# Kernel tuning notes

Measured on AMD Instinct MI355X. Metric: run time of the kernel, lower is better.

The kernel has to match this reference:

```python
import jax, jax.numpy as jnp
import numpy as np

B, C, F, TP = 16, 64, 128, 100
E = 576
NFEAT, NHID, NOUT = 128, 128, 64
RATIO = 0.9
BN_EPS = 1e-5


def setup_inputs() -> dict:
    key = jax.random.key(0)
    ks = jax.random.split(key, 16)
    s = 0.05
    h = jax.random.normal(ks[0], (B, C, F, TP), jnp.float32)
    edge_index = jax.random.randint(ks[1], (2, E), 0, C, dtype=jnp.int32)
    edge_weight = jax.random.uniform(ks[2], (E,), jnp.float32)
    W1 = jax.random.normal(ks[3], (NFEAT, NHID), jnp.float32) / np.float32(np.sqrt(NFEAT))
    b1 = s * jax.random.normal(ks[4], (NHID,), jnp.float32)
    g1 = 1.0 + s * jax.random.normal(ks[5], (NHID,), jnp.float32)
    be1 = s * jax.random.normal(ks[6], (NHID,), jnp.float32)
    a1 = jnp.full((1,), 0.25, jnp.float32)  # PReLU slope
    Wp = jax.random.normal(ks[7], (NHID, 1), jnp.float32) / np.float32(np.sqrt(NHID))
    bp = s * jax.random.normal(ks[8], (1,), jnp.float32)
    W2 = jax.random.normal(ks[9], (NHID, NOUT), jnp.float32) / np.float32(np.sqrt(NHID))
    b2 = s * jax.random.normal(ks[10], (NOUT,), jnp.float32)
    g2 = 1.0 + s * jax.random.normal(ks[11], (NOUT,), jnp.float32)
    be2 = s * jax.random.normal(ks[12], (NOUT,), jnp.float32)
    a2 = jnp.full((1,), 0.25, jnp.float32)
    return dict(h=h, edge_index=edge_index, edge_weight=edge_weight,
                W1=W1, b1=b1, g1=g1, be1=be1, a1=a1, Wp=Wp, bp=bp,
                W2=W2, b2=b2, g2=g2, be2=be2, a2=a2)


def gcn_conv(x, W, b, row, col, ew, N):
    # PyG GCNConv: add self-loops (weight 1), symmetric normalization, x@W, scatter-add to col.
    si = jnp.arange(N, dtype=row.dtype)
    r = jnp.concatenate([row, si])
    c = jnp.concatenate([col, si])
    w = jnp.concatenate([ew, jnp.ones((N,), x.dtype)])
    deg = jax.ops.segment_sum(w, c, num_segments=N)
    dis = jnp.where(deg > 0, jax.lax.rsqrt(jnp.maximum(deg, 1e-12)), 0.0)
    norm = dis[r] * w * dis[c]
    hlin = x @ W
    out = jax.ops.segment_sum(hlin[r] * norm[:, None], c, num_segments=N)
    return out + b


def batchnorm(x, g, beta):
    m = jnp.mean(x, axis=0)
    v = jnp.mean((x - m) ** 2, axis=0)  # biased var, as in torch BN training
    return (x - m) * jax.lax.rsqrt(v + BN_EPS) * g + beta


def prelu(x, a):
    return jnp.where(x >= 0, x, a * x)


def reference(h, edge_index, edge_weight, W1, b1, g1, be1, a1, Wp, bp, W2, b2, g2, be2, a2):
    Bv, Cv, Fv, Tpv = h.shape
    G = Bv * Tpv                      # num_graphs
    N = G * Cv                        # total nodes
    K = int(np.ceil(RATIO * Cv))      # kept nodes per graph (static)
    x = jnp.transpose(h, (0, 3, 1, 2)).reshape(N, Fv)
    Ev = edge_index.shape[1]
    offs = jnp.repeat(jnp.arange(G, dtype=edge_index.dtype) * Cv, Ev)
    row = jnp.tile(edge_index[0], G) + offs
    col = jnp.tile(edge_index[1], G) + offs
    ew = jnp.tile(edge_weight, G)
    # gc1 -> bn1 -> prelu
    x = prelu(batchnorm(gcn_conv(x, W1, b1, row, col, ew, N), g1, be1), a1)
    # SAGPooling: score GNN (GCNConv, no edge weights), tanh, per-graph top-k
    score = jnp.tanh(gcn_conv(x, Wp, bp, row, col, jnp.ones_like(ew), N)[:, 0])
    topv, topi = jax.lax.top_k(score.reshape(G, Cv), K)
    perm = (topi + (jnp.arange(G, dtype=topi.dtype) * Cv)[:, None]).reshape(-1)
    xk = x[perm] * topv.reshape(-1)[:, None]
    Nk = G * K
    new_id = jnp.zeros((N,), jnp.int32).at[perm].set(jnp.arange(Nk, dtype=jnp.int32))
    kept = jnp.zeros((N,), bool).at[perm].set(True)
    valid = kept[row] & kept[col]
    r2 = new_id[row]
    c2 = new_id[col]
    w2 = jnp.where(valid, ew, 0.0)    # dropped edges: weight 0 == filtered out
    # gc2 -> bn2 -> prelu (dropout is identity in eval)
    x2 = prelu(batchnorm(gcn_conv(xk, W2, b2, r2, c2, w2, Nk), g2, be2), a2)
    # global mean pool: exactly K nodes per graph, contiguous
    z = x2.reshape(G, K, -1).mean(axis=1)
    z_seq = jnp.transpose(z.reshape(Bv, Tpv, -1), (0, 2, 1))
    return x2, z_seq
```

## Files before the change

### kernel.cpp

```cpp
#include <hip/hip_runtime.h>

constexpr int Bc   = 16;
constexpr int Cc   = 64;
constexpr int Fc   = 128;
constexpr int TPc  = 100;
constexpr int Gc   = Bc * TPc;
constexpr int Nc   = Gc * Cc;
constexpr int Ec   = 576;
constexpr int NHID = 128;
constexpr int NOUTc= 64;
constexpr int Kc   = 58;
constexpr int Nkc  = Gc * Kc;

__global__ void k0_prep(const int* __restrict__ ei, const float* __restrict__ ew,
                        float* __restrict__ A1, float* __restrict__ AP,
                        double* bn1S, double* bn1Q, double* bn2S, double* bn2Q) {
    __shared__ float deg1[64], degP[64], dis1[64], disP[64];
    __shared__ float A1L[4096], APL[4096];
    int t = threadIdx.x;
    if (t < 64) { deg1[t] = 1.0f; degP[t] = 1.0f; }
    for (int i = t; i < 4096; i += 256) { A1L[i] = 0.f; APL[i] = 0.f; }
    if (t < 128) { bn1S[t] = 0.0; bn1Q[t] = 0.0; }
    if (t < 64)  { bn2S[t] = 0.0; bn2Q[t] = 0.0; }
    __syncthreads();
    for (int e = t; e < Ec; e += 256) {
        int c = ei[Ec + e];
        atomicAdd(&deg1[c], ew[e]);
        atomicAdd(&degP[c], 1.0f);
    }
    __syncthreads();
    if (t < 64) { dis1[t] = 1.0f / sqrtf(deg1[t]); disP[t] = 1.0f / sqrtf(degP[t]); }
    __syncthreads();
    for (int e = t; e < Ec; e += 256) {
        int r = ei[e], c = ei[Ec + e];
        atomicAdd(&A1L[c * 64 + r], dis1[r] * ew[e] * dis1[c]);
        atomicAdd(&APL[c * 64 + r], disP[r] * disP[c]);
    }
    __syncthreads();
    if (t < 64) {
        A1L[t * 65] += dis1[t] * dis1[t];
        APL[t * 65] += disP[t] * disP[t];
    }
    __syncthreads();
    for (int i = t; i < 4096; i += 256) { A1[i] = A1L[i]; AP[i] = APL[i]; }
}

__global__ __launch_bounds__(256)
void k_trans(const float* __restrict__ h, float* __restrict__ XT) {
    __shared__ float tile[64 * 101];
    int blk = blockIdx.x;
    int b = blk >> 7, f = blk & 127;
    int t = threadIdx.x;
    const float* hb = h + (size_t)b * 819200 + (size_t)f * 100;
    for (int i = t; i < 6400; i += 256) {
        unsigned c = (unsigned)i / 100u;
        unsigned tp = (unsigned)i - c * 100u;
        tile[c * 101 + tp] = hb[(size_t)c * 12800 + tp];
    }
    __syncthreads();
    float* xb = XT + (size_t)b * 100 * 8192 + f * 64;
    for (int j = t; j < 6400; j += 256) {
        int tp = j >> 6, c = j & 63;
        xb[(size_t)tp * 8192 + c] = tile[c * 101 + tp];
    }
}

__global__ __launch_bounds__(256, 2)
void k1_gc1(const float* __restrict__ XT, const float* __restrict__ W1,
            const float* __restrict__ b1, const float* __restrict__ A1,
            float* __restrict__ Y1, double* bn1S, double* bn1Q) {
    __shared__ float XsT[128 * 64];
    __shared__ float WH [64 * 128];
    __shared__ float A1s[4096];
    int g = blockIdx.x;
    int t = threadIdx.x;
    int tx = t & 31, ty = t >> 5;

    {
        const float4* src = (const float4*)(XT + (size_t)g * 8192);
        float4* dst = (float4*)XsT;
#pragma unroll
        for (int it = 0; it < 8; ++it) dst[it * 256 + t] = src[it * 256 + t];
    }
    for (int i = t; i < 4096; i += 256) A1s[i] = A1[i];

    float acc[8][4];
#pragma unroll
    for (int i = 0; i < 8; ++i)
#pragma unroll
        for (int j = 0; j < 4; ++j) acc[i][j] = 0.f;

    for (int kh = 0; kh < 2; ++kh) {
        __syncthreads();
        for (int it = 0; it < 32; ++it) {
            int e2 = it * 256 + t;
            int f = e2 & 127, kk = e2 >> 7;
            WH[kk * 128 + f] = W1[(kh * 64 + kk) * 128 + f];
        }
        __syncthreads();
        for (int kk = 0; kk < 64; ++kk) {
            int k = kh * 64 + kk;
            float4 x0 = *(const float4*)&XsT[k * 64 + ty * 8];
            float4 x1 = *(const float4*)&XsT[k * 64 + ty * 8 + 4];
            float4 w  = *(const float4*)&WH[kk * 128 + tx * 4];
            float xr[8] = {x0.x, x0.y, x0.z, x0.w, x1.x, x1.y, x1.z, x1.w};
#pragma unroll
            for (int i = 0; i < 8; ++i) {
                acc[i][0] += xr[i] * w.x;
                acc[i][1] += xr[i] * w.y;
                acc[i][2] += xr[i] * w.z;
                acc[i][3] += xr[i] * w.w;
            }
        }
    }
    __syncthreads();
#pragma unroll
    for (int i = 0; i < 8; ++i) {
        float4 v = make_float4(acc[i][0], acc[i][1], acc[i][2], acc[i][3]);
        *(float4*)&WH[(ty * 8 + i) * 128 + tx * 4] = v;
    }
    __syncthreads();
    float acy[8][4];
    float4 bb = *(const float4*)&b1[tx * 4];
#pragma unroll
    for (int i = 0; i < 8; ++i) { acy[i][0] = bb.x; acy[i][1] = bb.y; acy[i][2] = bb.z; acy[i][3] = bb.w; }
    for (int rr = 0; rr < 16; ++rr) {
        float4 hrow[4];
#pragma unroll
        for (int q = 0; q < 4; ++q) hrow[q] = *(const float4*)&WH[(rr * 4 + q) * 128 + tx * 4];
#pragma unroll
        for (int i = 0; i < 8; ++i) {
            float4 a4 = *(const float4*)&A1s[(ty * 8 + i) * 64 + rr * 4];
            acy[i][0] += a4.x * hrow[0].x + a4.y * hrow[1].x + a4.z * hrow[2].x + a4.w * hrow[3].x;
            acy[i][1] += a4.x * hrow[0].y + a4.y * hrow[1].y + a4.z * hrow[2].y + a4.w * hrow[3].y;
            acy[i][2] += a4.x * hrow[0].z + a4.y * hrow[1].z + a4.z * hrow[2].z + a4.w * hrow[3].z;
            acy[i][3] += a4.x * hrow[0].w + a4.y * hrow[1].w + a4.z * hrow[2].w + a4.w * hrow[3].w;
        }
    }
    float ps[4] = {0, 0, 0, 0}, pq[4] = {0, 0, 0, 0};
    float* Yg = Y1 + (size_t)g * 64 * 128;
#pragma unroll
    for (int i = 0; i < 8; ++i) {
        float4 v = make_float4(acy[i][0], acy[i][1], acy[i][2], acy[i][3]);
        *(float4*)&Yg[(ty * 8 + i) * 128 + tx * 4] = v;
#pragma unroll
        for (int j = 0; j < 4; ++j) { ps[j] += acy[i][j]; pq[j] += acy[i][j] * acy[i][j]; }
    }
    float* redS = XsT;
    float* redQ = XsT + 1024;
#pragma unroll
    for (int j = 0; j < 4; ++j) {
        redS[ty * 128 + tx * 4 + j] = ps[j];
        redQ[ty * 128 + tx * 4 + j] = pq[j];
    }
    __syncthreads();
    if (t < 128) {
        float S = 0.f, Q = 0.f;
        for (int y = 0; y < 8; ++y) { S += redS[y * 128 + t]; Q += redQ[y * 128 + t]; }
        atomicAdd(&bn1S[t], (double)S);
        atomicAdd(&bn1Q[t], (double)Q);
    }
}

__global__ void k_bnfin(const double* __restrict__ S, const double* __restrict__ Q,
                        const float* __restrict__ gam, const float* __restrict__ bet,
                        float* __restrict__ scale, float* __restrict__ shift, double invN) {
    int t = threadIdx.x;
    double m = S[t] * invN;
    double v = Q[t] * invN - m * m;
    double rstd = 1.0 / sqrt(v + 1e-5);
    float sc = (float)((double)gam[t] * rstd);
    scale[t] = sc;
    shift[t] = bet[t] - (float)m * sc;
}

__global__ __launch_bounds__(256, 2)
void k3_pool_gc2(const float* __restrict__ Y1, const float* __restrict__ scale1,
                 const float* __restrict__ shift1, const float* __restrict__ a1,
                 const float* __restrict__ Wp, const float* __restrict__ bp,
                 const float* __restrict__ AP, const int* __restrict__ ei,
                 const float* __restrict__ ew, const float* __restrict__ W2,
                 const float* __restrict__ b2,
                 float* __restrict__ Y2, double* bn2S, double* bn2Q) {
    __shared__ float Xs[64 * 132];
    __shared__ float A2s[4096];
    __shared__ float H2s[64 * 66];
    __shared__ float slin[64], psum[256], score[64], dis2[64], deg2[64];
    __shared__ int   rnk[64], ord[64];
    int g = blockIdx.x, t = threadIdx.x;
    int tx = t & 31, ty = t >> 5;
    float alpha1 = a1[0];

    const float* Yg = Y1 + (size_t)g * 8192;
    for (int it = 0; it < 32; ++it) {
        int e = it * 256 + t;
        int f = e & 127, c = e >> 7;
        float v = Yg[e] * scale1[f] + shift1[f];
        v = (v >= 0.f) ? v : alpha1 * v;
        Xs[c * 132 + f] = v;
    }
    __syncthreads();
    {
        int rr = t >> 2, q4 = t & 3;
        float sp = 0.f;
        for (int m = 0; m < 32; ++m) sp += Xs[rr * 132 + q4 * 32 + m] * Wp[q4 * 32 + m];
        psum[t] = sp;
    }
    __syncthreads();
    if (t < 64) slin[t] = psum[t * 4] + psum[t * 4 + 1] + psum[t * 4 + 2] + psum[t * 4 + 3];
    __syncthreads();
    if (t < 64) {
        float acc = bp[0];
        for (int r = 0; r < 64; ++r) acc += AP[t * 64 + r] * slin[r];
        score[t] = tanhf(acc);
    }
    __syncthreads();
    if (t < 64) {
        float sc = score[t];
        int cnt = 0;
        for (int c2 = 0; c2 < 64; ++c2) {
            float o = score[c2];
            cnt += (o > sc) || (o == sc && c2 < t);
        }
        rnk[t] = cnt;
        if (cnt < Kc) ord[cnt] = t;
    }
    for (int i = t; i < 4096; i += 256) A2s[i] = 0.f;
    if (t < 64) deg2[t] = 1.0f;
    __syncthreads();
    for (int e = t; e < Ec; e += 256) {
        int r = ei[e], c = ei[Ec + e];
        if (rnk[r] < Kc && rnk[c] < Kc) atomicAdd(&deg2[rnk[c]], ew[e]);
    }
    __syncthreads();
    if (t < 64) dis2[t] = 1.0f / sqrtf(deg2[t]);
    __syncthreads();
    for (int e = t; e < Ec; e += 256) {
        int r = ei[e], c = ei[Ec + e];
        int rkr = rnk[r], rkc = rnk[c];
        if (rkr < Kc && rkc < Kc) atomicAdd(&A2s[rkc * 64 + rkr], dis2[rkr] * ew[e] * dis2[rkc]);
    }
    __syncthreads();
    if (t < Kc) A2s[t * 65] += dis2[t] * dis2[t];
    __syncthreads();

    {
        int row0 = ty * 8;
        float acc2[8][2];
        int   cidx[8];
        float srow[8];
#pragma unroll
        for (int i = 0; i < 8; ++i) {
            acc2[i][0] = 0.f; acc2[i][1] = 0.f;
            int r = row0 + i;
            if (r < Kc) { cidx[i] = ord[r]; srow[i] = score[cidx[i]]; }
            else        { cidx[i] = 0;      srow[i] = 0.f; }
        }
        for (int k0 = 0; k0 < 128; k0 += 4) {
            float4 xv[8];
#pragma unroll
            for (int i = 0; i < 8; ++i) xv[i] = *(const float4*)&Xs[cidx[i] * 132 + k0];
#pragma unroll
            for (int q = 0; q < 4; ++q) {
                float2 w = *(const float2*)&W2[(k0 + q) * 64 + tx * 2];
#pragma unroll
                for (int i = 0; i < 8; ++i) {
                    float xq = (q == 0) ? xv[i].x : (q == 1) ? xv[i].y : (q == 2) ? xv[i].z : xv[i].w;
                    acc2[i][0] += xq * w.x;
                    acc2[i][1] += xq * w.y;
                }
            }
        }
#pragma unroll
        for (int i = 0; i < 8; ++i) {
            H2s[(row0 + i) * 66 + tx * 2]     = acc2[i][0] * srow[i];
            H2s[(row0 + i) * 66 + tx * 2 + 1] = acc2[i][1] * srow[i];
        }
    }
    __syncthreads();
    float acy[8][2];
    float2 b2v = *(const float2*)&b2[tx * 2];
#pragma unroll
    for (int i = 0; i < 8; ++i) { acy[i][0] = b2v.x; acy[i][1] = b2v.y; }
    for (int rr = 0; rr < 16; ++rr) {
        float2 h2[4];
#pragma unroll
        for (int q = 0; q < 4; ++q) h2[q] = *(const float2*)&H2s[(rr * 4 + q) * 66 + tx * 2];
#pragma unroll
        for (int i = 0; i < 8; ++i) {
            float4 a4 = *(const float4*)&A2s[(ty * 8 + i) * 64 + rr * 4];
            acy[i][0] += a4.x * h2[0].x + a4.y * h2[1].x + a4.z * h2[2].x + a4.w * h2[3].x;
            acy[i][1] += a4.x * h2[0].y + a4.y * h2[1].y + a4.z * h2[2].y + a4.w * h2[3].y;
        }
    }
    float s0 = 0.f, s1 = 0.f, q0 = 0.f, q1 = 0.f;
    float* Y2g = Y2 + (size_t)g * Kc * 64;
#pragma unroll
    for (int i = 0; i < 8; ++i) {
        int ck = ty * 8 + i;
        if (ck < Kc) {
            float2 v = make_float2(acy[i][0], acy[i][1]);
            *(float2*)&Y2g[ck * 64 + tx * 2] = v;
            s0 += v.x; s1 += v.y; q0 += v.x * v.x; q1 += v.y * v.y;
        }
    }
    float* redS = Xs;
    float* redQ = Xs + 512;
    redS[ty * 64 + tx * 2]     = s0;
    redS[ty * 64 + tx * 2 + 1] = s1;
    redQ[ty * 64 + tx * 2]     = q0;
    redQ[ty * 64 + tx * 2 + 1] = q1;
    __syncthreads();
    if (t < 64) {
        float S = 0.f, Q = 0.f;
        for (int y = 0; y < 8; ++y) { S += redS[y * 64 + t]; Q += redQ[y * 64 + t]; }
        atomicAdd(&bn2S[t], (double)S);
        atomicAdd(&bn2Q[t], (double)Q);
    }
}

__global__ void k5_out(const float* __restrict__ Y2, const float* __restrict__ scale2,
                       const float* __restrict__ shift2, const float* __restrict__ a2v,
                       float* __restrict__ out) {
    __shared__ float red[4 * 64];
    int g = blockIdx.x, t = threadIdx.x;
    float alpha = a2v[0];
    const float* Yg = Y2 + (size_t)g * Kc * 64;
    float* Og = out + (size_t)g * Kc * 64;
    int c = t & 63, rg = t >> 6;
    float part = 0.f;
    for (int rk = rg; rk < Kc; rk += 4) {
        float v = Yg[rk * 64 + c] * scale2[c] + shift2[c];
        v = (v >= 0.f) ? v : alpha * v;
        Og[rk * 64 + c] = v;
        part += v;
    }
    red[rg * 64 + c] = part;
    __syncthreads();
    if (t < 64) {
        float z = (red[t] + red[64 + t] + red[128 + t] + red[192 + t]) / (float)Kc;
        int b = g / TPc, tp = g % TPc;
        out[(size_t)Nkc * 64 + (size_t)b * NOUTc * TPc + t * TPc + tp] = z;
    }
}

extern "C" void kernel_launch(void* const* d_in, const int* in_sizes, int n_in,
                              void* d_out, int out_size, void* d_ws, size_t ws_size,
                              hipStream_t stream) {
    const float* h   = (const float*)d_in[0];
    const int*   ei  = (const int*)  d_in[1];
    const float* ew  = (const float*)d_in[2];
    const float* W1  = (const float*)d_in[3];
    const float* b1  = (const float*)d_in[4];
    const float* g1  = (const float*)d_in[5];
    const float* be1 = (const float*)d_in[6];
    const float* a1  = (const float*)d_in[7];
    const float* Wp  = (const float*)d_in[8];
    const float* bp  = (const float*)d_in[9];
    const float* W2  = (const float*)d_in[10];
    const float* b2  = (const float*)d_in[11];
    const float* g2  = (const float*)d_in[12];
    const float* be2 = (const float*)d_in[13];
    const float* a2  = (const float*)d_in[14];

    char* ws = (char*)d_ws;
    double* bn1S   = (double*)(ws + 0);
    double* bn1Q   = (double*)(ws + 1024);
    double* bn2S   = (double*)(ws + 2048);
    double* bn2Q   = (double*)(ws + 2560);
    float*  scale1 = (float*)(ws + 3072);
    float*  shift1 = (float*)(ws + 3584);
    float*  scale2 = (float*)(ws + 4096);
    float*  shift2 = (float*)(ws + 4352);
    float*  A1     = (float*)(ws + 4608);
    float*  AP     = (float*)(ws + 20992);
    float*  XT     = (float*)(ws + 37376);
    float*  Y1     = XT;
    float*  Y2     = (float*)(ws + 37376 + 52428800);
    float*  out    = (float*)d_out;

    hipLaunchKernelGGL(k0_prep, dim3(1), dim3(256), 0, stream,
                       ei, ew, A1, AP, bn1S, bn1Q, bn2S, bn2Q);
    hipLaunchKernelGGL(k_trans, dim3(2048), dim3(256), 0, stream, h, XT);
    hipLaunchKernelGGL(k1_gc1, dim3(Gc), dim3(256), 0, stream,
                       XT, W1, b1, A1, Y1, bn1S, bn1Q);
    hipLaunchKernelGGL(k_bnfin, dim3(1), dim3(128), 0, stream,
                       bn1S, bn1Q, g1, be1, scale1, shift1, 1.0 / (double)Nc);
    hipLaunchKernelGGL(k3_pool_gc2, dim3(Gc), dim3(256), 0, stream,
                       Y1, scale1, shift1, a1, Wp, bp, AP, ei, ew, W2, b2, Y2, bn2S, bn2Q);
    hipLaunchKernelGGL(k_bnfin, dim3(1), dim3(64), 0, stream,
                       bn2S, bn2Q, g2, be2, scale2, shift2, 1.0 / (double)Nkc);
    hipLaunchKernelGGL(k5_out, dim3(Gc), dim3(256), 0, stream,
                       Y2, scale2, shift2, a2, out);
}
```

Before: 230.0 us.

## Cut LDS footprint, index gc2 by original node order, raise occupancy

In gc1, the W1 tile is no longer staged in shared memory. W1 is read directly from global memory (cache-resident), and the XsT buffer is reused for the intermediate product, so shared memory per block drops and launch bounds rise to 3 blocks/SM. In the pool/gc2 kernel, the H2s and ord buffers are removed. The pooled GCN runs in original node index space, with rows remapped by rank only at the output store. AP is staged into shared memory with a rotated layout, edges are preloaded into registers, and input loads are vectorised. The aim is higher occupancy and less shared-memory traffic, at the cost of global/L2 reads of W1 in the inner loop and possible register pressure under the tighter launch bound.

```diff
diff --git a/kernel.cpp b/kernel.cpp
--- a/kernel.cpp
+++ b/kernel.cpp
@@ -65,15 +65,13 @@
     }
 }
 
-__global__ __launch_bounds__(256, 2)
+__global__ __launch_bounds__(256, 3)
 void k1_gc1(const float* __restrict__ XT, const float* __restrict__ W1,
             const float* __restrict__ b1, const float* __restrict__ A1,
             float* __restrict__ Y1, double* bn1S, double* bn1Q) {
-    __shared__ float XsT[128 * 64];
-    __shared__ float WH [64 * 128];
+    __shared__ float XsT[8192];
     __shared__ float A1s[4096];
-    int g = blockIdx.x;
-    int t = threadIdx.x;
+    int g = blockIdx.x, t = threadIdx.x;
     int tx = t & 31, ty = t >> 5;
 
     {
@@ -83,6 +81,7 @@
         for (int it = 0; it < 8; ++it) dst[it * 256 + t] = src[it * 256 + t];
     }
     for (int i = t; i < 4096; i += 256) A1s[i] = A1[i];
+    __syncthreads();
 
     float acc[8][4];
 #pragma unroll
@@ -90,34 +89,25 @@
 #pragma unroll
         for (int j = 0; j < 4; ++j) acc[i][j] = 0.f;
 
-    for (int kh = 0; kh < 2; ++kh) {
-        __syncthreads();
-        for (int it = 0; it < 32; ++it) {
-            int e2 = it * 256 + t;
-            int f = e2 & 127, kk = e2 >> 7;
-            WH[kk * 128 + f] = W1[(kh * 64 + kk) * 128 + f];
-        }
-        __syncthreads();
-        for (int kk = 0; kk < 64; ++kk) {
-            int k = kh * 64 + kk;
-            float4 x0 = *(const float4*)&XsT[k * 64 + ty * 8];
-            float4 x1 = *(const float4*)&XsT[k * 64 + ty * 8 + 4];
-            float4 w  = *(const float4*)&WH[kk * 128 + tx * 4];
-            float xr[8] = {x0.x, x0.y, x0.z, x0.w, x1.x, x1.y, x1.z, x1.w};
-#pragma unroll
-            for (int i = 0; i < 8; ++i) {
-                acc[i][0] += xr[i] * w.x;
-                acc[i][1] += xr[i] * w.y;
-                acc[i][2] += xr[i] * w.z;
-                acc[i][3] += xr[i] * w.w;
-            }
+#pragma unroll 4
+    for (int k = 0; k < 128; ++k) {
+        float4 x0 = *(const float4*)&XsT[k * 64 + ty * 8];
+        float4 x1 = *(const float4*)&XsT[k * 64 + ty * 8 + 4];
+        float4 w  = *(const float4*)&W1[k * 128 + tx * 4];
+        float xr[8] = {x0.x, x0.y, x0.z, x0.w, x1.x, x1.y, x1.z, x1.w};
+#pragma unroll
+        for (int i = 0; i < 8; ++i) {
+            acc[i][0] += xr[i] * w.x;
+            acc[i][1] += xr[i] * w.y;
+            acc[i][2] += xr[i] * w.z;
+            acc[i][3] += xr[i] * w.w;
         }
     }
     __syncthreads();
 #pragma unroll
     for (int i = 0; i < 8; ++i) {
         float4 v = make_float4(acc[i][0], acc[i][1], acc[i][2], acc[i][3]);
-        *(float4*)&WH[(ty * 8 + i) * 128 + tx * 4] = v;
+        *(float4*)&XsT[(ty * 8 + i) * 128 + tx * 4] = v;
     }
     __syncthreads();
     float acy[8][4];
@@ -127,7 +117,7 @@
     for (int rr = 0; rr < 16; ++rr) {
         float4 hrow[4];
 #pragma unroll
-        for (int q = 0; q < 4; ++q) hrow[q] = *(const float4*)&WH[(rr * 4 + q) * 128 + tx * 4];
+        for (int q = 0; q < 4; ++q) hrow[q] = *(const float4*)&XsT[(rr * 4 + q) * 128 + tx * 4];
 #pragma unroll
         for (int i = 0; i < 8; ++i) {
             float4 a4 = *(const float4*)&A1s[(ty * 8 + i) * 64 + rr * 4];
@@ -138,7 +128,7 @@
         }
     }
     float ps[4] = {0, 0, 0, 0}, pq[4] = {0, 0, 0, 0};
-    float* Yg = Y1 + (size_t)g * 64 * 128;
+    float* Yg = Y1 + (size_t)g * 8192;
 #pragma unroll
     for (int i = 0; i < 8; ++i) {
         float4 v = make_float4(acy[i][0], acy[i][1], acy[i][2], acy[i][3]);
@@ -146,6 +136,7 @@
 #pragma unroll
         for (int j = 0; j < 4; ++j) { ps[j] += acy[i][j]; pq[j] += acy[i][j] * acy[i][j]; }
     }
+    __syncthreads();
     float* redS = XsT;
     float* redQ = XsT + 1024;
 #pragma unroll
@@ -174,7 +165,7 @@
     shift[t] = bet[t] - (float)m * sc;
 }
 
-__global__ __launch_bounds__(256, 2)
+__global__ __launch_bounds__(256, 3)
 void k3_pool_gc2(const float* __restrict__ Y1, const float* __restrict__ scale1,
                  const float* __restrict__ shift1, const float* __restrict__ a1,
                  const float* __restrict__ Wp, const float* __restrict__ bp,
@@ -184,26 +175,48 @@
                  float* __restrict__ Y2, double* bn2S, double* bn2Q) {
     __shared__ float Xs[64 * 132];
     __shared__ float A2s[4096];
-    __shared__ float H2s[64 * 66];
     __shared__ float slin[64], psum[256], score[64], dis2[64], deg2[64];
-    __shared__ int   rnk[64], ord[64];
+    __shared__ int   rnk[64];
     int g = blockIdx.x, t = threadIdx.x;
     int tx = t & 31, ty = t >> 5;
     float alpha1 = a1[0];
 
-    const float* Yg = Y1 + (size_t)g * 8192;
-    for (int it = 0; it < 32; ++it) {
-        int e = it * 256 + t;
-        int f = e & 127, c = e >> 7;
-        float v = Yg[e] * scale1[f] + shift1[f];
-        v = (v >= 0.f) ? v : alpha1 * v;
-        Xs[c * 132 + f] = v;
+    int er0 = ei[t], ec0 = ei[Ec + t];           float wv0 = ew[t];
+    int er1 = ei[256 + t], ec1 = ei[Ec + 256 + t]; float wv1 = ew[256 + t];
+    int er2 = 0, ec2 = 0; float wv2 = 0.f;
+    if (t < Ec - 512) { er2 = ei[512 + t]; ec2 = ei[Ec + 512 + t]; wv2 = ew[512 + t]; }
+
+    {
+        float4 sc4 = *(const float4*)&scale1[tx * 4];
+        float4 sh4 = *(const float4*)&shift1[tx * 4];
+        const float4* Yg4 = (const float4*)(Y1 + (size_t)g * 8192);
+#pragma unroll
+        for (int it = 0; it < 8; ++it) {
+            float4 v = Yg4[it * 256 + t];
+            int c = (it * 256 + t) >> 5;
+            v.x = v.x * sc4.x + sh4.x; v.x = (v.x >= 0.f) ? v.x : alpha1 * v.x;
+            v.y = v.y * sc4.y + sh4.y; v.y = (v.y >= 0.f) ? v.y : alpha1 * v.y;
+            v.z = v.z * sc4.z + sh4.z; v.z = (v.z >= 0.f) ? v.z : alpha1 * v.z;
+            v.w = v.w * sc4.w + sh4.w; v.w = (v.w >= 0.f) ? v.w : alpha1 * v.w;
+            *(float4*)&Xs[c * 132 + tx * 4] = v;
+        }
+#pragma unroll
+        for (int k = 0; k < 16; ++k) {
+            int i = k * 256 + t;
+            int row = i >> 6, col = i & 63;
+            A2s[(row << 6) + ((col + row) & 63)] = AP[i];
+        }
     }
     __syncthreads();
     {
         int rr = t >> 2, q4 = t & 3;
         float sp = 0.f;
-        for (int m = 0; m < 32; ++m) sp += Xs[rr * 132 + q4 * 32 + m] * Wp[q4 * 32 + m];
+#pragma unroll
+        for (int m4 = 0; m4 < 8; ++m4) {
+            float4 x4 = *(const float4*)&Xs[rr * 132 + q4 * 32 + m4 * 4];
+            float4 w4 = *(const float4*)&Wp[q4 * 32 + m4 * 4];
+            sp += x4.x * w4.x + x4.y * w4.y + x4.z * w4.z + x4.w * w4.w;
+        }
         psum[t] = sp;
     }
     __syncthreads();
@@ -211,7 +224,8 @@
     __syncthreads();
     if (t < 64) {
         float acc = bp[0];
-        for (int r = 0; r < 64; ++r) acc += AP[t * 64 + r] * slin[r];
+#pragma unroll 8
+        for (int c = 0; c < 64; ++c) acc += A2s[(t << 6) + ((c + t) & 63)] * slin[c];
         score[t] = tanhf(acc);
     }
     __syncthreads();
@@ -223,43 +237,42 @@
             cnt += (o > sc) || (o == sc && c2 < t);
         }
         rnk[t] = cnt;
-        if (cnt < Kc) ord[cnt] = t;
-    }
-    for (int i = t; i < 4096; i += 256) A2s[i] = 0.f;
+    }
+    {
+        float4 z = make_float4(0.f, 0.f, 0.f, 0.f);
+        float4* A2s4 = (float4*)A2s;
+#pragma unroll
+        for (int j = 0; j < 4; ++j) A2s4[j * 256 + t] = z;
+    }
     if (t < 64) deg2[t] = 1.0f;
     __syncthreads();
-    for (int e = t; e < Ec; e += 256) {
-        int r = ei[e], c = ei[Ec + e];
-        if (rnk[r] < Kc && rnk[c] < Kc) atomicAdd(&deg2[rnk[c]], ew[e]);
-    }
-    __syncthreads();
-    if (t < 64) dis2[t] = 1.0f / sqrtf(deg2[t]);
-    __syncthreads();
-    for (int e = t; e < Ec; e += 256) {
-        int r = ei[e], c = ei[Ec + e];
-        int rkr = rnk[r], rkc = rnk[c];
-        if (rkr < Kc && rkc < Kc) atomicAdd(&A2s[rkc * 64 + rkr], dis2[rkr] * ew[e] * dis2[rkc]);
-    }
-    __syncthreads();
-    if (t < Kc) A2s[t * 65] += dis2[t] * dis2[t];
-    __syncthreads();
+    if (rnk[er0] < Kc && rnk[ec0] < Kc) atomicAdd(&deg2[ec0], wv0);
+    if (rnk[er1] < Kc && rnk[ec1] < Kc) atomicAdd(&deg2[ec1], wv1);
+    if (t < Ec - 512 && rnk[er2] < Kc && rnk[ec2] < Kc) atomicAdd(&deg2[ec2], wv2);
+    __syncthreads();
+    if (t < 64) dis2[t] = rsqrtf(deg2[t]);
+    __syncthreads();
+    if (rnk[er0] < Kc && rnk[ec0] < Kc) atomicAdd(&A2s[(ec0 << 6) + er0], dis2[er0] * wv0 * dis2[ec0]);
+    if (rnk[er1] < Kc && rnk[ec1] < Kc) atomicAdd(&A2s[(ec1 << 6) + er1], dis2[er1] * wv1 * dis2[ec1]);
+    if (t < Ec - 512 && rnk[er2] < Kc && rnk[ec2] < Kc) atomicAdd(&A2s[(ec2 << 6) + er2], dis2[er2] * wv2 * dis2[ec2]);
+    __syncthreads();
+    if (t < 64 && rnk[t] < Kc) A2s[t * 65] += dis2[t] * dis2[t];
 
     {
         int row0 = ty * 8;
         float acc2[8][2];
-        int   cidx[8];
         float srow[8];
 #pragma unroll
         for (int i = 0; i < 8; ++i) {
             acc2[i][0] = 0.f; acc2[i][1] = 0.f;
-            int r = row0 + i;
-            if (r < Kc) { cidx[i] = ord[r]; srow[i] = score[cidx[i]]; }
-            else        { cidx[i] = 0;      srow[i] = 0.f; }
-        }
+            int c = row0 + i;
+            srow[i] = (rnk[c] < Kc) ? score[c] : 0.f;
+        }
+#pragma unroll 2
         for (int k0 = 0; k0 < 128; k0 += 4) {
             float4 xv[8];
 #pragma unroll
-            for (int i = 0; i < 8; ++i) xv[i] = *(const float4*)&Xs[cidx[i] * 132 + k0];
+            for (int i = 0; i < 8; ++i) xv[i] = *(const float4*)&Xs[(row0 + i) * 132 + k0];
 #pragma unroll
             for (int q = 0; q < 4; ++q) {
                 float2 w = *(const float2*)&W2[(k0 + q) * 64 + tx * 2];
@@ -273,8 +286,8 @@
         }
 #pragma unroll
         for (int i = 0; i < 8; ++i) {
-            H2s[(row0 + i) * 66 + tx * 2]     = acc2[i][0] * srow[i];
-            H2s[(row0 + i) * 66 + tx * 2 + 1] = acc2[i][1] * srow[i];
+            *(float2*)&Xs[(row0 + i) * 132 + tx * 2] =
+                make_float2(acc2[i][0] * srow[i], acc2[i][1] * srow[i]);
         }
     }
     __syncthreads();
@@ -285,7 +298,7 @@
     for (int rr = 0; rr < 16; ++rr) {
         float2 h2[4];
 #pragma unroll
-        for (int q = 0; q < 4; ++q) h2[q] = *(const float2*)&H2s[(rr * 4 + q) * 66 + tx * 2];
+        for (int q = 0; q < 4; ++q) h2[q] = *(const float2*)&Xs[(rr * 4 + q) * 132 + tx * 2];
 #pragma unroll
         for (int i = 0; i < 8; ++i) {
             float4 a4 = *(const float4*)&A2s[(ty * 8 + i) * 64 + rr * 4];
@@ -297,13 +310,15 @@
     float* Y2g = Y2 + (size_t)g * Kc * 64;
 #pragma unroll
     for (int i = 0; i < 8; ++i) {
-        int ck = ty * 8 + i;
-        if (ck < Kc) {
-            float2 v = make_float2(acy[i][0], acy[i][1]);
-            *(float2*)&Y2g[ck * 64 + tx * 2] = v;
-            s0 += v.x; s1 += v.y; q0 += v.x * v.x; q1 += v.y * v.y;
-        }
-    }
+        int c = ty * 8 + i;
+        int rk = rnk[c];
+        if (rk < Kc) {
+            *(float2*)&Y2g[rk * 64 + tx * 2] = make_float2(acy[i][0], acy[i][1]);
+            s0 += acy[i][0]; s1 += acy[i][1];
+            q0 += acy[i][0] * acy[i][0]; q1 += acy[i][1] * acy[i][1];
+        }
+    }
+    __syncthreads();
     float* redS = Xs;
     float* redQ = Xs + 512;
     redS[ty * 64 + tx * 2]     = s0;
```

Result: slower. 581.3 us (+152.7%).

## Split pooling+GC2 kernel into two kernels passing H2 through global slab

Applied to the files above, without the earlier changes.

The fused pool/GC2 kernel is split in two. The first kernel computes scores, ranks and the scaled H2 = X[perm]@W2, and writes H2 plus the ranks back into the graph's own Y1 slab in place. The second kernel reloads that slab, builds the pooled adjacency and does the aggregation and BN statistics. Each kernel now uses less shared memory, which should allow more blocks per CU, at the cost of an extra launch and a global round trip of about 16KB per graph.

```diff
diff --git a/kernel.cpp b/kernel.cpp
--- a/kernel.cpp
+++ b/kernel.cpp
@@ -175,23 +175,19 @@
 }
 
 __global__ __launch_bounds__(256, 2)
-void k3_pool_gc2(const float* __restrict__ Y1, const float* __restrict__ scale1,
-                 const float* __restrict__ shift1, const float* __restrict__ a1,
-                 const float* __restrict__ Wp, const float* __restrict__ bp,
-                 const float* __restrict__ AP, const int* __restrict__ ei,
-                 const float* __restrict__ ew, const float* __restrict__ W2,
-                 const float* __restrict__ b2,
-                 float* __restrict__ Y2, double* bn2S, double* bn2Q) {
+void k3a_pool(float* __restrict__ Y1, const float* __restrict__ scale1,
+              const float* __restrict__ shift1, const float* __restrict__ a1,
+              const float* __restrict__ Wp, const float* __restrict__ bp,
+              const float* __restrict__ AP, const float* __restrict__ W2) {
     __shared__ float Xs[64 * 132];
-    __shared__ float A2s[4096];
-    __shared__ float H2s[64 * 66];
-    __shared__ float slin[64], psum[256], score[64], dis2[64], deg2[64];
+    __shared__ float slin[64], psum[256], score[64];
     __shared__ int   rnk[64], ord[64];
     int g = blockIdx.x, t = threadIdx.x;
     int tx = t & 31, ty = t >> 5;
     float alpha1 = a1[0];
 
-    const float* Yg = Y1 + (size_t)g * 8192;
+    float* slab = Y1 + (size_t)g * 8192;
+    const float* Yg = slab;
     for (int it = 0; it < 32; ++it) {
         int e = it * 256 + t;
         int f = e & 127, c = e >> 7;
@@ -224,24 +220,8 @@
         }
         rnk[t] = cnt;
         if (cnt < Kc) ord[cnt] = t;
-    }
-    for (int i = t; i < 4096; i += 256) A2s[i] = 0.f;
-    if (t < 64) deg2[t] = 1.0f;
-    __syncthreads();
-    for (int e = t; e < Ec; e += 256) {
-        int r = ei[e], c = ei[Ec + e];
-        if (rnk[r] < Kc && rnk[c] < Kc) atomicAdd(&deg2[rnk[c]], ew[e]);
-    }
-    __syncthreads();
-    if (t < 64) dis2[t] = 1.0f / sqrtf(deg2[t]);
-    __syncthreads();
-    for (int e = t; e < Ec; e += 256) {
-        int r = ei[e], c = ei[Ec + e];
-        int rkr = rnk[r], rkc = rnk[c];
-        if (rkr < Kc && rkc < Kc) atomicAdd(&A2s[rkc * 64 + rkr], dis2[rkr] * ew[e] * dis2[rkc]);
-    }
-    __syncthreads();
-    if (t < Kc) A2s[t * 65] += dis2[t] * dis2[t];
+        ((int*)(slab + 4096))[t] = cnt;
+    }
     __syncthreads();
 
     {
@@ -273,11 +253,58 @@
         }
 #pragma unroll
         for (int i = 0; i < 8; ++i) {
-            H2s[(row0 + i) * 66 + tx * 2]     = acc2[i][0] * srow[i];
-            H2s[(row0 + i) * 66 + tx * 2 + 1] = acc2[i][1] * srow[i];
-        }
-    }
-    __syncthreads();
+            *(float2*)&slab[(row0 + i) * 64 + tx * 2] =
+                make_float2(acc2[i][0] * srow[i], acc2[i][1] * srow[i]);
+        }
+    }
+}
+
+__global__ __launch_bounds__(256, 2)
+void k3b_gc2(const float* __restrict__ Y1, const int* __restrict__ ei,
+             const float* __restrict__ ew, const float* __restrict__ b2,
+             float* __restrict__ Y2, double* bn2S, double* bn2Q) {
+    __shared__ float H2s[64 * 68];
+    __shared__ float A2s[4096];
+    __shared__ float dis2[64], deg2[64];
+    __shared__ int   rnk[64];
+    int g = blockIdx.x, t = threadIdx.x;
+    int tx = t & 31, ty = t >> 5;
+
+    const float* slab = Y1 + (size_t)g * 8192;
+    {
+        const float4* src = (const float4*)slab;
+#pragma unroll
+        for (int it = 0; it < 4; ++it) {
+            int i4 = it * 256 + t;
+            int r = i4 >> 4, c4 = i4 & 15;
+            *(float4*)&H2s[r * 68 + c4 * 4] = src[i4];
+        }
+    }
+    if (t < 64) rnk[t] = ((const int*)(slab + 4096))[t];
+    {
+        float4 z = make_float4(0.f, 0.f, 0.f, 0.f);
+        float4* A2s4 = (float4*)A2s;
+#pragma unroll
+        for (int j = 0; j < 4; ++j) A2s4[j * 256 + t] = z;
+    }
+    if (t < 64) deg2[t] = 1.0f;
+    __syncthreads();
+    for (int e = t; e < Ec; e += 256) {
+        int r = ei[e], c = ei[Ec + e];
+        if (rnk[r] < Kc && rnk[c] < Kc) atomicAdd(&deg2[rnk[c]], ew[e]);
+    }
+    __syncthreads();
+    if (t < 64) dis2[t] = 1.0f / sqrtf(deg2[t]);
+    __syncthreads();
+    for (int e = t; e < Ec; e += 256) {
+        int r = ei[e], c = ei[Ec + e];
+        int rkr = rnk[r], rkc = rnk[c];
+        if (rkr < Kc && rkc < Kc) atomicAdd(&A2s[rkc * 64 + rkr], dis2[rkr] * ew[e] * dis2[rkc]);
+    }
+    __syncthreads();
+    if (t < Kc) A2s[t * 65] += dis2[t] * dis2[t];
+    __syncthreads();
+
     float acy[8][2];
     float2 b2v = *(const float2*)&b2[tx * 2];
 #pragma unroll
@@ -285,7 +312,7 @@
     for (int rr = 0; rr < 16; ++rr) {
         float2 h2[4];
 #pragma unroll
-        for (int q = 0; q < 4; ++q) h2[q] = *(const float2*)&H2s[(rr * 4 + q) * 66 + tx * 2];
+        for (int q = 0; q < 4; ++q) h2[q] = *(const float2*)&H2s[(rr * 4 + q) * 68 + tx * 2];
 #pragma unroll
         for (int i = 0; i < 8; ++i) {
             float4 a4 = *(const float4*)&A2s[(ty * 8 + i) * 64 + rr * 4];
@@ -304,8 +331,9 @@
             s0 += v.x; s1 += v.y; q0 += v.x * v.x; q1 += v.y * v.y;
         }
     }
-    float* redS = Xs;
-    float* redQ = Xs + 512;
+    __syncthreads();
+    float* redS = H2s;
+    float* redQ = H2s + 512;
     redS[ty * 64 + tx * 2]     = s0;
     redS[ty * 64 + tx * 2 + 1] = s1;
     redQ[ty * 64 + tx * 2]     = q0;
@@ -386,8 +414,10 @@
                        XT, W1, b1, A1, Y1, bn1S, bn1Q);
     hipLaunchKernelGGL(k_bnfin, dim3(1), dim3(128), 0, stream,
                        bn1S, bn1Q, g1, be1, scale1, shift1, 1.0 / (double)Nc);
-    hipLaunchKernelGGL(k3_pool_gc2, dim3(Gc), dim3(256), 0, stream,
-                       Y1, scale1, shift1, a1, Wp, bp, AP, ei, ew, W2, b2, Y2, bn2S, bn2Q);
+    hipLaunchKernelGGL(k3a_pool, dim3(Gc), dim3(256), 0, stream,
+                       Y1, scale1, shift1, a1, Wp, bp, AP, W2);
+    hipLaunchKernelGGL(k3b_gc2, dim3(Gc), dim3(256), 0, stream,
+                       Y1, ei, ew, b2, Y2, bn2S, bn2Q);
     hipLaunchKernelGGL(k_bnfin, dim3(1), dim3(64), 0, stream,
                        bn2S, bn2Q, g2, be2, scale2, shift2, 1.0 / (double)Nkc);
     hipLaunchKernelGGL(k5_out, dim3(Gc), dim3(256), 0, stream,
```

New measurement: 234.2 us. No clear change (+1.8%).
